# Performance work log

Measured on AMD Instinct MI355X. Metric: run time of the kernel, lower is better.

## Reference

```python
import jax, jax.numpy as jnp
import numpy as np

TEMPERATURE = 0.1
BASE_TEMPERATURE = 0.07
N = 8192
D = 128


def setup_inputs() -> dict:
    key = jax.random.key(0)
    kf, kl = jax.random.split(key)
    feats = jax.random.normal(kf, (N, 1, D), dtype=jnp.float32)
    # contrastive embeddings are typically L2-normalized upstream
    feats = feats / jnp.linalg.norm(feats, axis=-1, keepdims=True)
    labels = jax.random.randint(kl, (N,), 0, 2, dtype=jnp.int32)
    return {"feats": feats, "labels": labels}


def reference(feats, labels):
    # feats: [anchor_num, n_view=1, D]; labels: [anchor_num] binary fg/bg
    anchor_num, n_view, d = feats.shape
    n = anchor_num * n_view  # n_view == 1 in this module
    contrast_feature = feats.reshape(n, d)

    lab = labels.reshape(-1, 1)
    pos_mask = (lab == lab.T).astype(feats.dtype)  # [N, N]
    neg_mask = 1.0 - pos_mask

    # [N, N] similarity logits
    logits = jnp.matmul(contrast_feature, contrast_feature.T) / TEMPERATURE
    logits_max = jax.lax.stop_gradient(jnp.max(logits, axis=1, keepdims=True))
    logits = logits - logits_max

    # mask out self-contrast on the diagonal (logits_mask in torch code)
    idx = jnp.arange(n)
    pos_mask = pos_mask.at[idx, idx].set(0.0)

    exp_logits = jnp.exp(logits)
    neg_logits = jnp.sum(exp_logits * neg_mask, axis=1, keepdims=True)  # [N,1]
    log_prob = logits - jnp.log(exp_logits + neg_logits)

    mean_log_prob_pos = jnp.sum(pos_mask * log_prob, axis=1) / jnp.sum(pos_mask, axis=1)
    loss = -(TEMPERATURE / BASE_TEMPERATURE) * mean_log_prob_pos
    return jnp.mean(loss)
```

## Files before the change

kernel.cpp:

```cpp
#include <hip/hip_runtime.h>
#include <hip/hip_bf16.h>

#define NN 8192
#define DD 128

typedef short bf16x8 __attribute__((ext_vector_type(8)));
typedef float f32x4 __attribute__((ext_vector_type(4)));

#define LOG2E 1.4426950408889634f
#define K2f   14.426950408889634f

#define M_OFF    (NN * DD * 2)
#define LABF_OFF (M_OFF + NN * 4)
#define G_OFF    (LABF_OFF + NN * 4)
#define CNT_OFF  (G_OFF + 256 * 4)
#define EG_OFF   (CNT_OFF + 256)
#define ELG_OFF  (EG_OFF + NN * 4)

#define BROWS 256
#define BCOLS 512
#define TCOLS 32
#define ITERS (BCOLS / TCOLS)

__device__ __forceinline__ unsigned short f2bf(float x) {
    unsigned u = __float_as_uint(x);
    u = (u + 0x7FFFu + ((u >> 16) & 1u)) >> 16;
    return (unsigned short)u;
}

__global__ __launch_bounds__(256) void prep_kernel(const float* __restrict__ F,
        const int* __restrict__ labels, unsigned short* __restrict__ F16,
        float* __restrict__ M, float* __restrict__ labf, float* __restrict__ G,
        int* __restrict__ cnt1, float* __restrict__ Eg, float* __restrict__ Elg) {
    __shared__ float sG[256];
    __shared__ int scnt;
    const int tid = threadIdx.x;
    sG[tid] = 0.f;
    if (tid == 0) scnt = 0;
    __syncthreads();
    const int wave = tid >> 6, lane = tid & 63;
    const int half = lane >> 5, l32 = lane & 31;
    const int rb = blockIdx.x * 32;
    if (tid < 32) { Eg[rb + tid] = 0.f; Elg[rb + tid] = 0.f; }
    int mycnt = 0;
    float g1a[4] = {0.f, 0.f, 0.f, 0.f}, gta[4] = {0.f, 0.f, 0.f, 0.f};
    #pragma unroll
    for (int it = 0; it < 4; ++it) {
        const int row = rb + it * 8 + wave * 2 + half;
        const int lab = labels[row];
        const float lf = (float)lab;
        const float4 f = *reinterpret_cast<const float4*>(F + row * DD + l32 * 4);
        ushort4 u;
        u.x = f2bf(f.x); u.y = f2bf(f.y); u.z = f2bf(f.z); u.w = f2bf(f.w);
        *reinterpret_cast<ushort4*>(F16 + row * DD + l32 * 4) = u;
        g1a[0] = fmaf(lf, f.x, g1a[0]); gta[0] += f.x;
        g1a[1] = fmaf(lf, f.y, g1a[1]); gta[1] += f.y;
        g1a[2] = fmaf(lf, f.z, g1a[2]); gta[2] += f.z;
        g1a[3] = fmaf(lf, f.w, g1a[3]); gta[3] += f.w;
        float ss = fmaf(f.x, f.x, fmaf(f.y, f.y, fmaf(f.z, f.z, f.w * f.w)));
        #pragma unroll
        for (int off = 1; off < 32; off <<= 1) ss += __shfl_xor(ss, off);
        if (l32 == 0) {
            M[row] = 10.0f * ss;
            labf[row] = lf;
            mycnt += lab;
        }
    }
    #pragma unroll
    for (int j = 0; j < 4; ++j) {
        atomicAdd(&sG[l32 * 4 + j], g1a[j]);
        atomicAdd(&sG[128 + l32 * 4 + j], gta[j]);
    }
    if (l32 == 0 && mycnt) atomicAdd(&scnt, mycnt);
    __syncthreads();
    atomicAdd(&G[tid], sG[tid]);
    if (tid == 0) atomicAdd(cnt1, scnt);
}

__global__ __launch_bounds__(512, 4) void loss_kernel(
        const unsigned short* __restrict__ F16, const float* __restrict__ M,
        const float* __restrict__ labf, float* __restrict__ Eg,
        float* __restrict__ Elg) {
    __shared__ unsigned short Bt[2][TCOLS * DD];
    __shared__ float Lab[BCOLS];
    const int tid  = threadIdx.x;
    const int wave = tid >> 6, lane = tid & 63;
    const int quad = lane >> 4, l16 = lane & 15;
    const int rb = (blockIdx.x & 31) * BROWS;
    const int cb = (blockIdx.x >> 5) * BCOLS;

    Lab[tid] = labf[cb + tid];

    const int rw = rb + wave * 32;
    bf16x8 a[2][4];
    #pragma unroll
    for (int m = 0; m < 2; m++)
        #pragma unroll
        for (int kb = 0; kb < 4; kb++)
            a[m][kb] = *reinterpret_cast<const bf16x8*>(
                F16 + (rw + m * 16 + l16) * DD + kb * 32 + quad * 8);

    float mneg[2][4];
    #pragma unroll
    for (int m = 0; m < 2; m++)
        #pragma unroll
        for (int r = 0; r < 4; r++)
            mneg[m][r] = -M[rw + m * 16 + quad * 4 + r] * LOG2E;

    const int scol = tid >> 4;
    const int sc   = tid & 15;
    const unsigned short* sbase = F16 + (cb + scol) * DD + sc * 8;
    const int sdst = sc * (TCOLS * 8) + (((scol ^ sc) & 31) * 8);

    *reinterpret_cast<bf16x8*>(&Bt[0][sdst]) =
        *reinterpret_cast<const bf16x8*>(sbase);

    float accE[2][4] = {}, accEl[2][4] = {};
    __syncthreads();

    for (int it = 0; it < ITERS; ++it) {
        const int cur = it & 1;
        const int itn = (it + 1) & (ITERS - 1);
        const bf16x8 vn = *reinterpret_cast<const bf16x8*>(sbase + itn * TCOLS * DD);

        #pragma unroll
        for (int g = 0; g < 2; ++g) {
            bf16x8 bfr[4];
            #pragma unroll
            for (int kb = 0; kb < 4; kb++) {
                const int cr = kb * 4 + quad;
                const int col = g * 16 + l16;
                bfr[kb] = *reinterpret_cast<const bf16x8*>(
                    &Bt[cur][cr * (TCOLS * 8) + (((col ^ cr) & 31) * 8)]);
            }
            f32x4 d0 = {0.f, 0.f, 0.f, 0.f}, d1 = {0.f, 0.f, 0.f, 0.f};
            #pragma unroll
            for (int kb = 0; kb < 4; kb++) {
                d0 = __builtin_amdgcn_mfma_f32_16x16x32_bf16(a[0][kb], bfr[kb], d0, 0, 0, 0);
                d1 = __builtin_amdgcn_mfma_f32_16x16x32_bf16(a[1][kb], bfr[kb], d1, 0, 0, 0);
            }
            const float lc = Lab[it * TCOLS + g * 16 + l16];
            #pragma unroll
            for (int m = 0; m < 2; m++) {
                #pragma unroll
                for (int r = 0; r < 4; r++) {
                    const float vv = (m == 0) ? d0[r] : d1[r];
                    const float e = exp2f(fmaf(vv, K2f, mneg[m][r]));
                    accE[m][r] += e;
                    accEl[m][r] = fmaf(lc, e, accEl[m][r]);
                }
            }
        }

        *reinterpret_cast<bf16x8*>(&Bt[cur ^ 1][sdst]) = vn;
        __syncthreads();
    }

    #pragma unroll
    for (int m = 0; m < 2; m++) {
        #pragma unroll
        for (int r = 0; r < 4; r++) {
            float e = accE[m][r], el = accEl[m][r];
            #pragma unroll
            for (int off = 1; off < 16; off <<= 1) {
                e  += __shfl_xor(e,  off);
                el += __shfl_xor(el, off);
            }
            if (l16 == 0) {
                const int row = rw + m * 16 + quad * 4 + r;
                atomicAdd(&Eg[row], e);
                atomicAdd(&Elg[row], el);
            }
        }
    }
}

__global__ __launch_bounds__(256) void final_kernel(
        const unsigned short* __restrict__ F16, const float* __restrict__ M,
        const int* __restrict__ labels, const float* __restrict__ G,
        const int* __restrict__ cnt1, const float* __restrict__ Eg,
        const float* __restrict__ Elg, float* __restrict__ out) {
    __shared__ float sG[256];
    __shared__ float wsum[4];
    const int tid = threadIdx.x;
    sG[tid] = G[tid];
    __syncthreads();
    const int row = blockIdx.x * 256 + tid;
    const int lr = labels[row];
    float dot = 0.f;
    const unsigned short* f = F16 + row * DD;
    #pragma unroll
    for (int k = 0; k < DD; k += 8) {
        const bf16x8 fv = *reinterpret_cast<const bf16x8*>(f + k);
        #pragma unroll
        for (int j = 0; j < 8; j++) {
            const float fj = __uint_as_float(((unsigned)(unsigned short)fv[j]) << 16);
            const float g1 = sG[k + j];
            const float gl = lr ? g1 : (sG[128 + k + j] - g1);
            dot = fmaf(fj, gl, dot);
        }
    }
    const float E    = Eg[row];
    const float El   = Elg[row];
    const float Epos = lr ? El : (E - El);
    const float Si   = E - Epos;
    const float mi   = M[row];
    const int   c1   = *cnt1;
    const float cntp1 = (float)(lr ? c1 : (NN - c1));
    const float cnt   = cntp1 - 1.f;
    const float sum_l   = fmaf(10.f, dot, -cntp1 * mi);
    const float sum_log = cntp1 * __logf(Si) + Epos / Si;
    float li = -(10.f / 7.f) * (sum_l - sum_log) / cnt;
    #pragma unroll
    for (int off = 1; off < 64; off <<= 1) li += __shfl_xor(li, off);
    if ((tid & 63) == 0) wsum[tid >> 6] = li;
    __syncthreads();
    if (tid == 0)
        atomicAdd(out, (wsum[0] + wsum[1] + wsum[2] + wsum[3]) * (1.0f / NN));
}

extern "C" void kernel_launch(void* const* d_in, const int* in_sizes, int n_in,
                              void* d_out, int out_size, void* d_ws, size_t ws_size,
                              hipStream_t stream) {
    const float* F      = (const float*)d_in[0];
    const int*   labels = (const int*)d_in[1];
    float*       out    = (float*)d_out;
    char*        ws     = (char*)d_ws;
    unsigned short* F16 = (unsigned short*)ws;
    float*       M      = (float*)(ws + M_OFF);
    float*       labf   = (float*)(ws + LABF_OFF);
    float*       G      = (float*)(ws + G_OFF);
    int*         cnt1   = (int*)(ws + CNT_OFF);
    float*       Eg     = (float*)(ws + EG_OFF);
    float*       Elg    = (float*)(ws + ELG_OFF);

    hipMemsetAsync(out, 0, sizeof(float), stream);
    hipMemsetAsync(ws + G_OFF, 0, 256 * 4 + 256, stream);

    prep_kernel<<<NN / 32, 256, 0, stream>>>(F, labels, F16, M, labf, G, cnt1, Eg, Elg);
    loss_kernel<<<512, 512, 0, stream>>>(F16, M, labf, Eg, Elg);
    final_kernel<<<NN / 256, 256, 0, stream>>>(F16, M, labels, G, cnt1, Eg, Elg, out);
}
```

Baseline: 106.5 us.

## Repack bf16 features into k-chunk-major layout and load B fragments directly from global

The prep kernel now writes the bf16 features in a layout where each 8-element k-chunk is contiguous across rows, so MFMA A and B fragments can be loaded straight from global memory with coalesced 16-byte loads. The loss kernel drops its shared-memory B tile staging, the column-label LDS array and the per-iteration __syncthreads, and instead double-buffers B fragments in registers. Each wave now fetches its own B data, which relies on L2/L1 serving repeated loads in place of shared-memory reuse across the eight waves. The final kernel reads the original fp32 features instead of the bf16 copy for the dot product.

```diff
diff --git a/kernel.cpp b/kernel.cpp
--- a/kernel.cpp
+++ b/kernel.cpp
@@ -17,11 +17,6 @@
 #define EG_OFF   (CNT_OFF + 256)
 #define ELG_OFF  (EG_OFF + NN * 4)
 
-#define BROWS 256
-#define BCOLS 512
-#define TCOLS 32
-#define ITERS (BCOLS / TCOLS)
-
 __device__ __forceinline__ unsigned short f2bf(float x) {
     unsigned u = __float_as_uint(x);
     u = (u + 0x7FFFu + ((u >> 16) & 1u)) >> 16;
@@ -29,7 +24,7 @@
 }
 
 __global__ __launch_bounds__(256) void prep_kernel(const float* __restrict__ F,
-        const int* __restrict__ labels, unsigned short* __restrict__ F16,
+        const int* __restrict__ labels, unsigned short* __restrict__ P,
         float* __restrict__ M, float* __restrict__ labf, float* __restrict__ G,
         int* __restrict__ cnt1, float* __restrict__ Eg, float* __restrict__ Elg) {
     __shared__ float sG[256];
@@ -44,6 +39,7 @@
     if (tid < 32) { Eg[rb + tid] = 0.f; Elg[rb + tid] = 0.f; }
     int mycnt = 0;
     float g1a[4] = {0.f, 0.f, 0.f, 0.f}, gta[4] = {0.f, 0.f, 0.f, 0.f};
+    const int ch = l32 >> 1, hh = l32 & 1;
     #pragma unroll
     for (int it = 0; it < 4; ++it) {
         const int row = rb + it * 8 + wave * 2 + half;
@@ -52,7 +48,7 @@
         const float4 f = *reinterpret_cast<const float4*>(F + row * DD + l32 * 4);
         ushort4 u;
         u.x = f2bf(f.x); u.y = f2bf(f.y); u.z = f2bf(f.z); u.w = f2bf(f.w);
-        *reinterpret_cast<ushort4*>(F16 + row * DD + l32 * 4) = u;
+        *reinterpret_cast<ushort4*>(P + ((size_t)ch * NN + row) * 8 + hh * 4) = u;
         g1a[0] = fmaf(lf, f.x, g1a[0]); gta[0] += f.x;
         g1a[1] = fmaf(lf, f.y, g1a[1]); gta[1] += f.y;
         g1a[2] = fmaf(lf, f.z, g1a[2]); gta[2] += f.z;
@@ -78,27 +74,23 @@
 }
 
 __global__ __launch_bounds__(512, 4) void loss_kernel(
-        const unsigned short* __restrict__ F16, const float* __restrict__ M,
+        const unsigned short* __restrict__ P, const float* __restrict__ M,
         const float* __restrict__ labf, float* __restrict__ Eg,
         float* __restrict__ Elg) {
-    __shared__ unsigned short Bt[2][TCOLS * DD];
-    __shared__ float Lab[BCOLS];
     const int tid  = threadIdx.x;
     const int wave = tid >> 6, lane = tid & 63;
     const int quad = lane >> 4, l16 = lane & 15;
-    const int rb = (blockIdx.x & 31) * BROWS;
-    const int cb = (blockIdx.x >> 5) * BCOLS;
-
-    Lab[tid] = labf[cb + tid];
-
+    const int rb = (blockIdx.x & 31) * 256;
+    const int cb = (blockIdx.x >> 5) * 512;
     const int rw = rb + wave * 32;
+
     bf16x8 a[2][4];
     #pragma unroll
     for (int m = 0; m < 2; m++)
         #pragma unroll
         for (int kb = 0; kb < 4; kb++)
             a[m][kb] = *reinterpret_cast<const bf16x8*>(
-                F16 + (rw + m * 16 + l16) * DD + kb * 32 + quad * 8);
+                P + ((size_t)(kb * 4 + quad) * NN + rw + m * 16 + l16) * 8);
 
     float mneg[2][4];
     #pragma unroll
@@ -107,53 +99,45 @@
         for (int r = 0; r < 4; r++)
             mneg[m][r] = -M[rw + m * 16 + quad * 4 + r] * LOG2E;
 
-    const int scol = tid >> 4;
-    const int sc   = tid & 15;
-    const unsigned short* sbase = F16 + (cb + scol) * DD + sc * 8;
-    const int sdst = sc * (TCOLS * 8) + (((scol ^ sc) & 31) * 8);
-
-    *reinterpret_cast<bf16x8*>(&Bt[0][sdst]) =
-        *reinterpret_cast<const bf16x8*>(sbase);
+    const unsigned short* pB = P + ((size_t)quad * NN + cb + l16) * 8;
+    const float* pL = labf + cb + l16;
+
+    bf16x8 bb[2][4];
+    #pragma unroll
+    for (int kb = 0; kb < 4; kb++)
+        bb[0][kb] = *reinterpret_cast<const bf16x8*>(pB + (size_t)kb * 4 * NN * 8);
+    float lcur = pL[0];
 
     float accE[2][4] = {}, accEl[2][4] = {};
-    __syncthreads();
-
-    for (int it = 0; it < ITERS; ++it) {
-        const int cur = it & 1;
-        const int itn = (it + 1) & (ITERS - 1);
-        const bf16x8 vn = *reinterpret_cast<const bf16x8*>(sbase + itn * TCOLS * DD);
-
-        #pragma unroll
-        for (int g = 0; g < 2; ++g) {
-            bf16x8 bfr[4];
+
+    #pragma unroll 4
+    for (int it = 0; it < 32; ++it) {
+        const int cur = it & 1, nxt = cur ^ 1;
+        const int itn = (it + 1) & 31;
+        #pragma unroll
+        for (int kb = 0; kb < 4; kb++)
+            bb[nxt][kb] = *reinterpret_cast<const bf16x8*>(
+                pB + (size_t)kb * 4 * NN * 8 + itn * 128);
+        const float lnxt = pL[itn * 16];
+
+        f32x4 d0 = {0.f, 0.f, 0.f, 0.f}, d1 = {0.f, 0.f, 0.f, 0.f};
+        #pragma unroll
+        for (int kb = 0; kb < 4; kb++) {
+            d0 = __builtin_amdgcn_mfma_f32_16x16x32_bf16(a[0][kb], bb[cur][kb], d0, 0, 0, 0);
+            d1 = __builtin_amdgcn_mfma_f32_16x16x32_bf16(a[1][kb], bb[cur][kb], d1, 0, 0, 0);
+        }
+
+        #pragma unroll
+        for (int m = 0; m < 2; m++) {
             #pragma unroll
-            for (int kb = 0; kb < 4; kb++) {
-                const int cr = kb * 4 + quad;
-                const int col = g * 16 + l16;
-                bfr[kb] = *reinterpret_cast<const bf16x8*>(
-                    &Bt[cur][cr * (TCOLS * 8) + (((col ^ cr) & 31) * 8)]);
+            for (int r = 0; r < 4; r++) {
+                const float vv = (m == 0) ? d0[r] : d1[r];
+                const float e = exp2f(fmaf(vv, K2f, mneg[m][r]));
+                accE[m][r] += e;
+                accEl[m][r] = fmaf(lcur, e, accEl[m][r]);
             }
-            f32x4 d0 = {0.f, 0.f, 0.f, 0.f}, d1 = {0.f, 0.f, 0.f, 0.f};
-            #pragma unroll
-            for (int kb = 0; kb < 4; kb++) {
-                d0 = __builtin_amdgcn_mfma_f32_16x16x32_bf16(a[0][kb], bfr[kb], d0, 0, 0, 0);
-                d1 = __builtin_amdgcn_mfma_f32_16x16x32_bf16(a[1][kb], bfr[kb], d1, 0, 0, 0);
-            }
-            const float lc = Lab[it * TCOLS + g * 16 + l16];
-            #pragma unroll
-            for (int m = 0; m < 2; m++) {
-                #pragma unroll
-                for (int r = 0; r < 4; r++) {
-                    const float vv = (m == 0) ? d0[r] : d1[r];
-                    const float e = exp2f(fmaf(vv, K2f, mneg[m][r]));
-                    accE[m][r] += e;
-                    accEl[m][r] = fmaf(lc, e, accEl[m][r]);
-                }
-            }
-        }
-
-        *reinterpret_cast<bf16x8*>(&Bt[cur ^ 1][sdst]) = vn;
-        __syncthreads();
+        }
+        lcur = lnxt;
     }
 
     #pragma unroll
@@ -176,7 +160,7 @@
 }
 
 __global__ __launch_bounds__(256) void final_kernel(
-        const unsigned short* __restrict__ F16, const float* __restrict__ M,
+        const float* __restrict__ F, const float* __restrict__ M,
         const int* __restrict__ labels, const float* __restrict__ G,
         const int* __restrict__ cnt1, const float* __restrict__ Eg,
         const float* __restrict__ Elg, float* __restrict__ out) {
@@ -188,13 +172,13 @@
     const int row = blockIdx.x * 256 + tid;
     const int lr = labels[row];
     float dot = 0.f;
-    const unsigned short* f = F16 + row * DD;
-    #pragma unroll
-    for (int k = 0; k < DD; k += 8) {
-        const bf16x8 fv = *reinterpret_cast<const bf16x8*>(f + k);
-        #pragma unroll
-        for (int j = 0; j < 8; j++) {
-            const float fj = __uint_as_float(((unsigned)(unsigned short)fv[j]) << 16);
+    const float* f = F + (size_t)row * DD;
+    #pragma unroll
+    for (int k = 0; k < DD; k += 4) {
+        const float4 fv = *reinterpret_cast<const float4*>(f + k);
+        #pragma unroll
+        for (int j = 0; j < 4; j++) {
+            const float fj = (&fv.x)[j];
             const float g1 = sG[k + j];
             const float gl = lr ? g1 : (sG[128 + k + j] - g1);
             dot = fmaf(fj, gl, dot);
@@ -226,7 +210,7 @@
     const int*   labels = (const int*)d_in[1];
     float*       out    = (float*)d_out;
     char*        ws     = (char*)d_ws;
-    unsigned short* F16 = (unsigned short*)ws;
+    unsigned short* P   = (unsigned short*)ws;
     float*       M      = (float*)(ws + M_OFF);
     float*       labf   = (float*)(ws + LABF_OFF);
     float*       G      = (float*)(ws + G_OFF);
@@ -237,7 +221,7 @@
     hipMemsetAsync(out, 0, sizeof(float), stream);
     hipMemsetAsync(ws + G_OFF, 0, 256 * 4 + 256, stream);
 
-    prep_kernel<<<NN / 32, 256, 0, stream>>>(F, labels, F16, M, labf, G, cnt1, Eg, Elg);
-    loss_kernel<<<512, 512, 0, stream>>>(F16, M, labf, Eg, Elg);
-    final_kernel<<<NN / 256, 256, 0, stream>>>(F16, M, labels, G, cnt1, Eg, Elg, out);
-}
+    prep_kernel<<<NN / 32, 256, 0, stream>>>(F, labels, P, M, labf, G, cnt1, Eg, Elg);
+    loss_kernel<<<512, 512, 0, stream>>>(P, M, labf, Eg, Elg);
+    final_kernel<<<NN / 256, 256, 0, stream>>>(F, M, labels, G, cnt1, Eg, Elg, out);
+}
```

Result: slower. 110.3 us (+3.5%).
